# Kernel optimization log

Hardware: AMD Instinct MI355X
Metric: run time of the kernel (lower is better)

Reference implementation:

```python
import jax, jax.numpy as jnp
import numpy as np

NUM_HEADS = 4
HIDDEN = 128
LN_EPS = 1e-6
NEG_INF = -1e9


def setup_inputs() -> dict:
    key = jax.random.key(0)
    ks = jax.random.split(key, 8)
    B, S, H, NH = 64, 512, HIDDEN, NUM_HEADS
    enc = jax.random.normal(ks[0], (B, S, H), dtype=jnp.float32)
    mask = jax.random.randint(ks[1], (B, 1, S, S), 0, 2, dtype=jnp.int32)
    scale = 1.0 / np.sqrt(H)
    # torch Linear(H, H*NH, bias=False): weight is (H*NH, H); store transposed (H, H*NH)
    Wq = jax.random.normal(ks[2], (H, H * NH), dtype=jnp.float32) * scale
    Wk = jax.random.normal(ks[3], (H, H * NH), dtype=jnp.float32) * scale
    Wv = jax.random.normal(ks[4], (H, H * NH), dtype=jnp.float32) * scale
    Wo = jax.random.normal(ks[5], (H * NH, H), dtype=jnp.float32) * (1.0 / np.sqrt(H * NH))
    gamma = jnp.ones((H,), dtype=jnp.float32)
    beta = jnp.zeros((H,), dtype=jnp.float32)
    return {"enc": enc, "mask": mask, "Wq": Wq, "Wk": Wk, "Wv": Wv, "Wo": Wo, "gamma": gamma, "beta": beta}


def reference(enc, mask, Wq, Wk, Wv, Wo, gamma, beta):
    B, S, H = enc.shape
    NH = NUM_HEADS
    # projections -> (B, NH, S, H): each head has head_dim == hidden_units
    Q = (enc @ Wq).reshape(B, S, NH, H).transpose(0, 2, 1, 3)
    K = (enc @ Wk).reshape(B, S, NH, H).transpose(0, 2, 1, 3)
    V = (enc @ Wv).reshape(B, S, NH, H).transpose(0, 2, 1, 3)
    # scaled dot-product attention with mask (non-flash: full score matrix)
    scores = jnp.einsum('bhqd,bhkd->bhqk', Q, K) / jnp.sqrt(jnp.float32(H))
    scores = jnp.where(mask == 0, jnp.float32(NEG_INF), scores)
    attn = jax.nn.softmax(scores, axis=-1)  # dropout = identity in eval mode
    ctx = jnp.einsum('bhqk,bhkd->bhqd', attn, V)  # (B, NH, S, H)
    ctx = ctx.transpose(0, 2, 1, 3).reshape(B, S, NH * H)
    out = ctx @ Wo + enc  # dropout identity, residual add
    # LayerNorm over last dim
    mu = jnp.mean(out, axis=-1, keepdims=True)
    var = jnp.var(out, axis=-1, keepdims=True)
    return gamma * (out - mu) / jnp.sqrt(var + LN_EPS) + beta
```

## Files before the change

### kernel.cpp

```cpp
#include <hip/hip_runtime.h>
#include <stdint.h>

#define BATCH 64
#define SLEN 512
#define HID 128
#define NHEAD 4
#define DPROJ 512
#define MTOT (BATCH * SLEN)
#define SCALE 0.08838834764831845f
#define LOG2E 1.4426950408889634f

using short8 = __attribute__((ext_vector_type(8))) short;
using f32x4  = __attribute__((ext_vector_type(4))) float;
using u32x4  = __attribute__((ext_vector_type(4))) unsigned int;
using u32x2  = __attribute__((ext_vector_type(2))) unsigned int;
using us4    = __attribute__((ext_vector_type(4))) unsigned short;

__device__ __forceinline__ unsigned short f2bf(float f) {
  unsigned int u = __float_as_uint(f);
  u += 0x7fffu + ((u >> 16) & 1u);
  return (unsigned short)(u >> 16);
}

__global__ __launch_bounds__(256) void prep_kernel(
    const float* __restrict__ Wq,
    const float* __restrict__ Wk,
    const float* __restrict__ Wv,
    const float* __restrict__ Wo,
    const float* __restrict__ enc,
    const int* __restrict__ mask,
    unsigned short* __restrict__ WT,
    unsigned short* __restrict__ WoT,
    unsigned short* __restrict__ encb,
    unsigned int* __restrict__ mbits)
{
  if (blockIdx.x < 1024) {
    int idx = blockIdx.x * 256 + threadIdx.x;
    int z = idx >> 16;
    int i = idx & 65535;
    if (z < 3) {
      const float* W = (z == 0) ? Wq : (z == 1) ? Wk : Wv;
      float scale = (z == 0) ? (SCALE * LOG2E) : 1.0f;
      int k = i >> 9;
      int n = i & 511;
      WT[(size_t)z * 65536 + (size_t)n * 128 + k] = f2bf(W[i] * scale);
    } else {
      int k = i >> 7;
      int n = i & 127;
      WoT[(size_t)n * 512 + k] = f2bf(Wo[i]);
    }
  } else if (blockIdx.x < 3072) {
    size_t tid = (size_t)(blockIdx.x - 1024) * 256 + threadIdx.x;
    const float* s = enc + tid * 8;
    f32x4 a0 = *(const f32x4*)(s);
    f32x4 a1 = *(const f32x4*)(s + 4);
    short8 v;
    #pragma unroll
    for (int j = 0; j < 4; ++j) v[j] = (short)f2bf(a0[j]);
    #pragma unroll
    for (int j = 0; j < 4; ++j) v[4 + j] = (short)f2bf(a1[j]);
    *(short8*)(encb + tid * 8) = v;
  } else {
    const int l = threadIdx.x & 63;
    size_t wavebase = (size_t)(blockIdx.x - 3072) * 1024 + (threadIdx.x >> 6) * 256;
    unsigned long long b0 = __ballot(mask[wavebase + 0 * 64 + l] != 0);
    unsigned long long b1 = __ballot(mask[wavebase + 1 * 64 + l] != 0);
    unsigned long long b2 = __ballot(mask[wavebase + 2 * 64 + l] != 0);
    unsigned long long b3 = __ballot(mask[wavebase + 3 * 64 + l] != 0);
    if (l < 4) {
      unsigned long long v = (l & 2) ? ((l & 1) ? b3 : b2) : ((l & 1) ? b1 : b0);
      *(unsigned long long*)(mbits + (wavebase >> 5) + l * 2) = v;
    }
  }
}

__global__ __launch_bounds__(256) void qkv_kernel(
    const unsigned short* __restrict__ encb,
    const unsigned short* __restrict__ WT,
    unsigned short* __restrict__ Qh,
    unsigned short* __restrict__ Kh,
    unsigned short* __restrict__ Vt)
{
  const int nt = blockIdx.x;
  const int mt = blockIdx.y;
  const int t = threadIdx.x;
  const int lane = t & 63;
  const int w = t >> 6;
  const int quad = lane >> 4;
  const int l16 = lane & 15;

  __shared__ __align__(16) unsigned short Ald[128 * 136];
  __shared__ __align__(16) unsigned short Bld[2][128 * 72];

  const int m0 = mt * 128, n0 = nt * 128;
  const int wm = (w >> 1) * 64, wn = (w & 1) * 64;

  const int b_row = t >> 3, b_col = (t & 7) << 3;

  {
    u32x4 areg[8];
    #pragma unroll
    for (int i = 0; i < 8; ++i) {
      int idx = i * 256 + t;
      areg[i] = *(const u32x4*)(encb + (size_t)(m0 + (idx >> 4)) * HID + ((idx & 15) << 3));
    }
    u32x4 breg0[4];
    #pragma unroll
    for (int i = 0; i < 4; ++i)
      breg0[i] = *(const u32x4*)(WT + (size_t)(n0 + b_row + i * 32) * HID + b_col);
    #pragma unroll
    for (int i = 0; i < 8; ++i) {
      int idx = i * 256 + t;
      *(u32x4*)(Ald + (idx >> 4) * 136 + ((idx & 15) << 3)) = areg[i];
    }
    #pragma unroll
    for (int i = 0; i < 4; ++i)
      *(u32x4*)(Bld[0] + (b_row + i * 32) * 72 + b_col) = breg0[i];
  }
  u32x4 breg[4];
  #pragma unroll
  for (int i = 0; i < 4; ++i)
    breg[i] = *(const u32x4*)(WT + (size_t)(n0 + b_row + i * 32) * HID + 64 + b_col);
  asm volatile("s_waitcnt lgkmcnt(0)" ::: "memory");
  __builtin_amdgcn_s_barrier();

  f32x4 acc[4][4];
  #pragma unroll
  for (int s = 0; s < 6; ++s) {
    const int z = s >> 1, kc = s & 1, p = s & 1;
    if (kc == 0) {
      #pragma unroll
      for (int mi = 0; mi < 4; ++mi)
        #pragma unroll
        for (int ni = 0; ni < 4; ++ni)
          acc[mi][ni] = f32x4{0.f, 0.f, 0.f, 0.f};
    }

    const unsigned short* Br = Bld[p];
    #pragma unroll
    for (int kk = 0; kk < 2; ++kk) {
      short8 a[4], bb[4];
      #pragma unroll
      for (int mi = 0; mi < 4; ++mi)
        a[mi] = *(const short8*)(Ald + (wm + mi * 16 + l16) * 136 + kc * 64 + kk * 32 + quad * 8);
      #pragma unroll
      for (int ni = 0; ni < 4; ++ni)
        bb[ni] = *(const short8*)(Br + (wn + ni * 16 + l16) * 72 + kk * 32 + quad * 8);
      if (z < 2) {
        #pragma unroll
        for (int mi = 0; mi < 4; ++mi)
          #pragma unroll
          for (int ni = 0; ni < 4; ++ni)
            acc[mi][ni] = __builtin_amdgcn_mfma_f32_16x16x32_bf16(bb[ni], a[mi], acc[mi][ni], 0, 0, 0);
      } else {
        #pragma unroll
        for (int mi = 0; mi < 4; ++mi)
          #pragma unroll
          for (int ni = 0; ni < 4; ++ni)
            acc[mi][ni] = __builtin_amdgcn_mfma_f32_16x16x32_bf16(a[mi], bb[ni], acc[mi][ni], 0, 0, 0);
      }
    }

    if (s < 5) {
      unsigned short* Bw2 = Bld[p ^ 1];
      #pragma unroll
      for (int i = 0; i < 4; ++i)
        *(u32x4*)(Bw2 + (b_row + i * 32) * 72 + b_col) = breg[i];
      if (s < 4) {
        const int s2 = s + 2;
        const unsigned short* Wz = WT + (size_t)(s2 >> 1) * DPROJ * HID;
        #pragma unroll
        for (int i = 0; i < 4; ++i)
          breg[i] = *(const u32x4*)(Wz + (size_t)(n0 + b_row + i * 32) * HID + (s2 & 1) * 64 + b_col);
      }
      asm volatile("s_waitcnt lgkmcnt(0)" ::: "memory");
      __builtin_amdgcn_s_barrier();
    }

    if (kc == 1) {
      if (z < 2) {
        unsigned short* outz = ((z == 0) ? Qh : Kh) + (size_t)nt * MTOT * HID;
        #pragma unroll
        for (int mi = 0; mi < 4; ++mi)
          #pragma unroll
          for (int ni = 0; ni < 4; ++ni) {
            int m = m0 + wm + mi * 16 + l16;
            int dbase = wn + ni * 16 + quad * 4;
            us4 pk;
            #pragma unroll
            for (int r = 0; r < 4; ++r) pk[r] = f2bf(acc[mi][ni][r]);
            *(us4*)(outz + (size_t)m * HID + dbase) = pk;
          }
      } else {
        #pragma unroll
        for (int mi = 0; mi < 4; ++mi)
          #pragma unroll
          for (int ni = 0; ni < 4; ++ni) {
            int row0 = m0 + wm + mi * 16 + quad * 4;
            int b = row0 >> 9, sres = row0 & 511;
            int d = wn + ni * 16 + l16;
            us4 pk;
            #pragma unroll
            for (int r = 0; r < 4; ++r) pk[r] = f2bf(acc[mi][ni][r]);
            *(us4*)(Vt + ((size_t)(nt * BATCH + b) * HID + d) * SLEN + sres) = pk;
          }
      }
    }
  }
}

__global__ __launch_bounds__(512, 4) void attn_kernel(
    const unsigned short* __restrict__ Qh,
    const unsigned short* __restrict__ Kh,
    const unsigned short* __restrict__ Vt,
    const unsigned int* __restrict__ mbits,
    unsigned short* __restrict__ ctx)
{
  const int lin = blockIdx.x;
  const int work = (lin & 7) * 128 + (lin >> 3);
  const int qt = work & 3;
  const int h  = (work >> 2) & 3;
  const int b  = work >> 4;

  const int t = threadIdx.x;
  const int lane = t & 63;
  const int w = t >> 6;
  const int quad = lane >> 4;
  const int l16 = lane & 15;

  __shared__ __align__(16) unsigned short Kld[2][64 * 136];
  __shared__ __align__(16) unsigned short Vtld[2][128 * 72];

  const int q0 = qt * 128;
  const size_t rowbase = (size_t)b * SLEN;
  const unsigned short* kbase0 = Kh + ((size_t)h * MTOT + rowbase) * HID;
  const unsigned short* vbase  = Vt + (size_t)(h * BATCH + b) * HID * SLEN;
  const unsigned int* mrow = mbits + (size_t)b * SLEN * 16;

  const int k_key = t >> 4, k_col = (t & 15) << 3;
  const int v_d   = t >> 3, v_cc  = (t & 7) << 3;

  short8 qa[4];
  {
    const unsigned short* qbase =
        Qh + ((size_t)h * MTOT + rowbase + q0 + w * 16 + l16) * HID + quad * 8;
    #pragma unroll
    for (int kk = 0; kk < 4; ++kk)
      qa[kk] = *(const short8*)(qbase + kk * 32);
  }

  short8 ones;
  #pragma unroll
  for (int j = 0; j < 8; ++j) ones[j] = (short)0x3F80;

  f32x4 oc[8], oc9;
  #pragma unroll
  for (int nd = 0; nd < 8; ++nd) oc[nd] = f32x4{0.f, 0.f, 0.f, 0.f};
  oc9 = f32x4{0.f, 0.f, 0.f, 0.f};

  const unsigned int* mq = mrow + (size_t)(q0 + w * 16 + l16) * 16;

  u32x4 kreg[2], vreg[2];
  #pragma unroll
  for (int i = 0; i < 2; ++i) {
    kreg[i] = *(const u32x4*)(kbase0 + (size_t)(k_key + i * 32) * HID + k_col);
    vreg[i] = *(const u32x4*)(vbase + (size_t)(v_d + i * 64) * SLEN + v_cc);
  }
  #pragma unroll
  for (int i = 0; i < 2; ++i) {
    *(u32x4*)(Kld[0] + (k_key + i * 32) * 136 + k_col) = kreg[i];
    *(u32x4*)(Vtld[0] + (v_d + i * 64) * 72 + v_cc) = vreg[i];
  }
  #pragma unroll
  for (int i = 0; i < 2; ++i) {
    kreg[i] = *(const u32x4*)(kbase0 + (size_t)(64 + k_key + i * 32) * HID + k_col);
    vreg[i] = *(const u32x4*)(vbase + (size_t)(v_d + i * 64) * SLEN + 64 + v_cc);
  }
  asm volatile("s_waitcnt lgkmcnt(0)" ::: "memory");
  __builtin_amdgcn_s_barrier();

  for (int c0 = 0; c0 < SLEN; c0 += 64) {
    const int p = (c0 >> 6) & 1;
    const unsigned short* Kr = Kld[p];
    const unsigned short* Vr = Vtld[p];

    if (c0 + 64 < SLEN) {
      unsigned short* Kw = Kld[p ^ 1];
      unsigned short* Vw = Vtld[p ^ 1];
      #pragma unroll
      for (int i = 0; i < 2; ++i) {
        *(u32x4*)(Kw + (k_key + i * 32) * 136 + k_col) = kreg[i];
        *(u32x4*)(Vw + (v_d + i * 64) * 72 + v_cc) = vreg[i];
      }
      if (c0 + 128 < SLEN) {
        #pragma unroll
        for (int i = 0; i < 2; ++i) {
          kreg[i] = *(const u32x4*)(kbase0 + (size_t)(c0 + 128 + k_key + i * 32) * HID + k_col);
          vreg[i] = *(const u32x4*)(vbase + (size_t)(v_d + i * 64) * SLEN + c0 + 128 + v_cc);
        }
      }
    }

    u32x2 mw = *(const u32x2*)(mq + (c0 >> 5));

    f32x4 sc[4];
    #pragma unroll
    for (int ni = 0; ni < 4; ++ni) sc[ni] = f32x4{0.f, 0.f, 0.f, 0.f};
    __builtin_amdgcn_s_setprio(1);
    #pragma unroll
    for (int kk = 0; kk < 4; ++kk) {
      #pragma unroll
      for (int ni = 0; ni < 4; ++ni) {
        short8 bb = *(const short8*)(Kr + (ni * 16 + l16) * 136 + kk * 32 + quad * 8);
        sc[ni] = __builtin_amdgcn_mfma_f32_16x16x32_bf16(bb, qa[kk], sc[ni], 0, 0, 0);
      }
    }
    __builtin_amdgcn_s_setprio(0);

    unsigned int pk[4][2];
    #pragma unroll
    for (int ni = 0; ni < 4; ++ni) {
      unsigned wsel = (ni < 2) ? mw[0] : mw[1];
      float pp[4];
      #pragma unroll
      for (int r = 0; r < 4; ++r) {
        int bit = (ni & 1) * 16 + quad * 4 + r;
        float e = __builtin_amdgcn_exp2f(sc[ni][r]);
        pp[r] = ((wsel >> bit) & 1u) ? e : 0.f;
      }
      asm("v_cvt_pk_bf16_f32 %0, %1, %2" : "=v"(pk[ni][0]) : "v"(pp[0]), "v"(pp[1]));
      asm("v_cvt_pk_bf16_f32 %0, %1, %2" : "=v"(pk[ni][1]) : "v"(pp[2]), "v"(pp[3]));
    }

    #pragma unroll
    for (int kb = 0; kb < 2; ++kb) {
      unsigned int c0w = pk[kb * 2][0], c2w = pk[kb * 2 + 1][0];
      asm("v_permlane32_swap_b32 %0, %1" : "+v"(c0w), "+v"(c2w));
      asm("v_permlane16_swap_b32 %0, %1" : "+v"(c0w), "+v"(c2w));
      unsigned int c1w = pk[kb * 2][1], c3w = pk[kb * 2 + 1][1];
      asm("v_permlane32_swap_b32 %0, %1" : "+v"(c1w), "+v"(c3w));
      asm("v_permlane16_swap_b32 %0, %1" : "+v"(c1w), "+v"(c3w));
      short8 a = __builtin_bit_cast(short8, u32x4{c0w, c1w, c2w, c3w});
      __builtin_amdgcn_s_setprio(1);
      #pragma unroll
      for (int nd = 0; nd < 8; ++nd) {
        short8 bv = *(const short8*)(Vr + (nd * 16 + l16) * 72 + kb * 32 + quad * 8);
        oc[nd] = __builtin_amdgcn_mfma_f32_16x16x32_bf16(a, bv, oc[nd], 0, 0, 0);
      }
      oc9 = __builtin_amdgcn_mfma_f32_16x16x32_bf16(a, ones, oc9, 0, 0, 0);
      __builtin_amdgcn_s_setprio(0);
    }

    if (c0 + 64 < SLEN) {
      asm volatile("s_waitcnt lgkmcnt(0)" ::: "memory");
      __builtin_amdgcn_s_barrier();
    }
  }

  float rcp[4];
  #pragma unroll
  for (int r = 0; r < 4; ++r) rcp[r] = __builtin_amdgcn_rcpf(oc9[r]);
  #pragma unroll
  for (int nd = 0; nd < 8; ++nd)
    #pragma unroll
    for (int r = 0; r < 4; ++r) {
      float val = oc[nd][r] * rcp[r];
      int row = q0 + w * 16 + quad * 4 + r;
      int col = h * HID + nd * 16 + l16;
      ctx[(rowbase + row) * DPROJ + col] = f2bf(val);
    }
}

__global__ __launch_bounds__(256, 2) void oproj_ln_kernel(
    const unsigned short* __restrict__ ctx,
    const unsigned short* __restrict__ WoT,
    const float* __restrict__ enc,
    const float* __restrict__ gamma,
    const float* __restrict__ beta,
    float* __restrict__ out)
{
  const int m0 = blockIdx.x * 64;
  const int t = threadIdx.x;
  const int lane = t & 63;
  const int w = t >> 6;
  const int quad = lane >> 4;
  const int l16 = lane & 15;

  __shared__ __align__(16) unsigned short Actx[2][64 * 72];
  __shared__ __align__(16) unsigned short Bw[2][128 * 72];

  const int a_row = t >> 3, a_col = (t & 7) << 3;
  const int b_row = t >> 3, b_col = (t & 7) << 3;

  f32x4 acc[8];
  #pragma unroll
  for (int ni = 0; ni < 8; ++ni) acc[ni] = f32x4{0.f, 0.f, 0.f, 0.f};

  u32x4 areg[2], breg[4];
  #pragma unroll
  for (int i = 0; i < 2; ++i)
    areg[i] = *(const u32x4*)(ctx + (size_t)(m0 + a_row + i * 32) * DPROJ + a_col);
  #pragma unroll
  for (int i = 0; i < 4; ++i)
    breg[i] = *(const u32x4*)(WoT + (size_t)(b_row + i * 32) * DPROJ + b_col);
  #pragma unroll
  for (int i = 0; i < 2; ++i)
    *(u32x4*)(Actx[0] + (a_row + i * 32) * 72 + a_col) = areg[i];
  #pragma unroll
  for (int i = 0; i < 4; ++i)
    *(u32x4*)(Bw[0] + (b_row + i * 32) * 72 + b_col) = breg[i];
  #pragma unroll
  for (int i = 0; i < 2; ++i)
    areg[i] = *(const u32x4*)(ctx + (size_t)(m0 + a_row + i * 32) * DPROJ + 64 + a_col);
  #pragma unroll
  for (int i = 0; i < 4; ++i)
    breg[i] = *(const u32x4*)(WoT + (size_t)(b_row + i * 32) * DPROJ + 64 + b_col);
  asm volatile("s_waitcnt lgkmcnt(0)" ::: "memory");
  __builtin_amdgcn_s_barrier();

  #pragma unroll
  for (int it = 0; it < 8; ++it) {
    const int p = it & 1;
    const unsigned short* Ar = Actx[p];
    const unsigned short* Br = Bw[p];
    #pragma unroll
    for (int kk = 0; kk < 2; ++kk) {
      short8 a = *(const short8*)(Ar + (w * 16 + l16) * 72 + kk * 32 + quad * 8);
      #pragma unroll
      for (int ni = 0; ni < 8; ++ni) {
        short8 bb = *(const short8*)(Br + (ni * 16 + l16) * 72 + kk * 32 + quad * 8);
        acc[ni] = __builtin_amdgcn_mfma_f32_16x16x32_bf16(a, bb, acc[ni], 0, 0, 0);
      }
    }
    if (it < 7) {
      unsigned short* Aw2 = Actx[p ^ 1];
      unsigned short* Bw2 = Bw[p ^ 1];
      #pragma unroll
      for (int i = 0; i < 2; ++i)
        *(u32x4*)(Aw2 + (a_row + i * 32) * 72 + a_col) = areg[i];
      #pragma unroll
      for (int i = 0; i < 4; ++i)
        *(u32x4*)(Bw2 + (b_row + i * 32) * 72 + b_col) = breg[i];
      if (it < 6) {
        const int kc2 = (it + 2) * 64;
        #pragma unroll
        for (int i = 0; i < 2; ++i)
          areg[i] = *(const u32x4*)(ctx + (size_t)(m0 + a_row + i * 32) * DPROJ + kc2 + a_col);
        #pragma unroll
        for (int i = 0; i < 4; ++i)
          breg[i] = *(const u32x4*)(WoT + (size_t)(b_row + i * 32) * DPROJ + kc2 + b_col);
      }
      asm volatile("s_waitcnt lgkmcnt(0)" ::: "memory");
      __builtin_amdgcn_s_barrier();
    }
  }

  float g[8], be[8];
  #pragma unroll
  for (int ni = 0; ni < 8; ++ni) {
    g[ni] = gamma[ni * 16 + l16];
    be[ni] = beta[ni * 16 + l16];
  }

  float val[8][4];
  #pragma unroll
  for (int r = 0; r < 4; ++r) {
    int m = m0 + w * 16 + quad * 4 + r;
    const float* erow = enc + (size_t)m * HID;
    float s = 0.f, s2 = 0.f;
    #pragma unroll
    for (int ni = 0; ni < 8; ++ni) {
      float v = acc[ni][r] + erow[ni * 16 + l16];
      val[ni][r] = v;
      s += v;
      s2 += v * v;
    }
    #pragma unroll
    for (int off = 1; off < 16; off <<= 1) {
      s  += __shfl_xor(s, off, 64);
      s2 += __shfl_xor(s2, off, 64);
    }
    float mean = s * (1.f / 128.f);
    float var = s2 * (1.f / 128.f) - mean * mean;
    float rstd = rsqrtf(var + 1e-6f);
    float* orow = out + (size_t)m * HID;
    #pragma unroll
    for (int ni = 0; ni < 8; ++ni)
      orow[ni * 16 + l16] = g[ni] * (val[ni][r] - mean) * rstd + be[ni];
  }
}

extern "C" void kernel_launch(void* const* d_in, const int* in_sizes, int n_in,
                              void* d_out, int out_size, void* d_ws, size_t ws_size,
                              hipStream_t stream) {
  const float* enc   = (const float*)d_in[0];
  const int*   mask  = (const int*)d_in[1];
  const float* Wq    = (const float*)d_in[2];
  const float* Wk    = (const float*)d_in[3];
  const float* Wv    = (const float*)d_in[4];
  const float* Wo    = (const float*)d_in[5];
  const float* gamma = (const float*)d_in[6];
  const float* beta  = (const float*)d_in[7];
  float* out = (float*)d_out;

  unsigned short* WT  = (unsigned short*)d_ws;
  unsigned short* WoT = WT + (size_t)3 * DPROJ * HID;
  unsigned short* Qh  = WoT + (size_t)HID * DPROJ;
  unsigned short* Kh  = Qh + (size_t)NHEAD * MTOT * HID;
  unsigned short* Vt  = Kh + (size_t)NHEAD * MTOT * HID;
  unsigned short* ctx = Vt + (size_t)NHEAD * MTOT * HID;
  unsigned short* encb = ctx + (size_t)MTOT * DPROJ;
  unsigned int* mbits = (unsigned int*)(encb + (size_t)MTOT * HID * 2);

  prep_kernel<<<19456, 256, 0, stream>>>(Wq, Wk, Wv, Wo, enc, mask, WT, WoT, encb, mbits);
  qkv_kernel<<<dim3(4, 256), 256, 0, stream>>>(encb, WT, Qh, Kh, Vt);
  attn_kernel<<<1024, 512, 0, stream>>>(Qh, Kh, Vt, mbits, ctx);
  oproj_ln_kernel<<<MTOT / 64, 256, 0, stream>>>(ctx, WoT, enc, gamma, beta, out);
}
```

Before: 222.9 us.

## Fuse enc bf16 conversion and mask bit-packing into the QKV kernel

The fp32-to-bf16 conversion of enc now happens inside the QKV GEMM's A-tile load, so the intermediate encb buffer is no longer written and read back. Mask bit-packing moves into extra blocks of the QKV launch, with each block looping over 32 chunks. The prep kernel now only transposes the weights. This saves a round trip of enc through global memory and lets mask packing overlap with the GEMM, at the cost of reading fp32 enc (twice as many bytes) in each of the 4 n-tiles and making the mask blocks longer-running.

New measurement: 232.9 us. 4.5% more time.

```diff
diff --git a/kernel.cpp b/kernel.cpp
--- a/kernel.cpp
+++ b/kernel.cpp
@@ -27,63 +27,58 @@
     const float* __restrict__ Wk,
     const float* __restrict__ Wv,
     const float* __restrict__ Wo,
+    unsigned short* __restrict__ WT,
+    unsigned short* __restrict__ WoT)
+{
+  int idx = blockIdx.x * 256 + threadIdx.x;
+  int z = idx >> 16;
+  int i = idx & 65535;
+  if (z < 3) {
+    const float* W = (z == 0) ? Wq : (z == 1) ? Wk : Wv;
+    float scale = (z == 0) ? (SCALE * LOG2E) : 1.0f;
+    int k = i >> 9;
+    int n = i & 511;
+    WT[(size_t)z * 65536 + (size_t)n * 128 + k] = f2bf(W[i] * scale);
+  } else {
+    int k = i >> 7;
+    int n = i & 127;
+    WoT[(size_t)n * 512 + k] = f2bf(Wo[i]);
+  }
+}
+
+__global__ __launch_bounds__(256) void qkv_kernel(
     const float* __restrict__ enc,
     const int* __restrict__ mask,
-    unsigned short* __restrict__ WT,
-    unsigned short* __restrict__ WoT,
-    unsigned short* __restrict__ encb,
-    unsigned int* __restrict__ mbits)
-{
-  if (blockIdx.x < 1024) {
-    int idx = blockIdx.x * 256 + threadIdx.x;
-    int z = idx >> 16;
-    int i = idx & 65535;
-    if (z < 3) {
-      const float* W = (z == 0) ? Wq : (z == 1) ? Wk : Wv;
-      float scale = (z == 0) ? (SCALE * LOG2E) : 1.0f;
-      int k = i >> 9;
-      int n = i & 511;
-      WT[(size_t)z * 65536 + (size_t)n * 128 + k] = f2bf(W[i] * scale);
-    } else {
-      int k = i >> 7;
-      int n = i & 127;
-      WoT[(size_t)n * 512 + k] = f2bf(Wo[i]);
-    }
-  } else if (blockIdx.x < 3072) {
-    size_t tid = (size_t)(blockIdx.x - 1024) * 256 + threadIdx.x;
-    const float* s = enc + tid * 8;
-    f32x4 a0 = *(const f32x4*)(s);
-    f32x4 a1 = *(const f32x4*)(s + 4);
-    short8 v;
-    #pragma unroll
-    for (int j = 0; j < 4; ++j) v[j] = (short)f2bf(a0[j]);
-    #pragma unroll
-    for (int j = 0; j < 4; ++j) v[4 + j] = (short)f2bf(a1[j]);
-    *(short8*)(encb + tid * 8) = v;
-  } else {
-    const int l = threadIdx.x & 63;
-    size_t wavebase = (size_t)(blockIdx.x - 3072) * 1024 + (threadIdx.x >> 6) * 256;
-    unsigned long long b0 = __ballot(mask[wavebase + 0 * 64 + l] != 0);
-    unsigned long long b1 = __ballot(mask[wavebase + 1 * 64 + l] != 0);
-    unsigned long long b2 = __ballot(mask[wavebase + 2 * 64 + l] != 0);
-    unsigned long long b3 = __ballot(mask[wavebase + 3 * 64 + l] != 0);
-    if (l < 4) {
-      unsigned long long v = (l & 2) ? ((l & 1) ? b3 : b2) : ((l & 1) ? b1 : b0);
-      *(unsigned long long*)(mbits + (wavebase >> 5) + l * 2) = v;
-    }
-  }
-}
-
-__global__ __launch_bounds__(256) void qkv_kernel(
-    const unsigned short* __restrict__ encb,
     const unsigned short* __restrict__ WT,
     unsigned short* __restrict__ Qh,
     unsigned short* __restrict__ Kh,
-    unsigned short* __restrict__ Vt)
+    unsigned short* __restrict__ Vt,
+    unsigned int* __restrict__ mbits)
 {
-  const int nt = blockIdx.x;
-  const int mt = blockIdx.y;
+  const int bid = blockIdx.x;
   const int t = threadIdx.x;
+
+  if (bid >= 1024) {
+    const int l = t & 63;
+    const int wv = t >> 6;
+    #pragma unroll 4
+    for (int it = 0; it < 32; ++it) {
+      size_t vb = (size_t)(bid - 1024) * 32 + it;
+      size_t wavebase = vb * 1024 + (size_t)wv * 256;
+      unsigned long long b0 = __ballot(mask[wavebase + 0 * 64 + l] != 0);
+      unsigned long long b1 = __ballot(mask[wavebase + 1 * 64 + l] != 0);
+      unsigned long long b2 = __ballot(mask[wavebase + 2 * 64 + l] != 0);
+      unsigned long long b3 = __ballot(mask[wavebase + 3 * 64 + l] != 0);
+      if (l < 4) {
+        unsigned long long v = (l & 2) ? ((l & 1) ? b3 : b2) : ((l & 1) ? b1 : b0);
+        *(unsigned long long*)(mbits + (wavebase >> 5) + l * 2) = v;
+      }
+    }
+    return;
+  }
+
+  const int nt = bid & 3;
+  const int mt = bid >> 2;
   const int lane = t & 63;
   const int w = t >> 6;
   const int quad = lane >> 4;
@@ -98,20 +93,24 @@
   const int b_row = t >> 3, b_col = (t & 7) << 3;
 
   {
-    u32x4 areg[8];
+    u32x4 breg0[4];
+    #pragma unroll
+    for (int i = 0; i < 4; ++i)
+      breg0[i] = *(const u32x4*)(WT + (size_t)(n0 + b_row + i * 32) * HID + b_col);
     #pragma unroll
     for (int i = 0; i < 8; ++i) {
       int idx = i * 256 + t;
-      areg[i] = *(const u32x4*)(encb + (size_t)(m0 + (idx >> 4)) * HID + ((idx & 15) << 3));
-    }
-    u32x4 breg0[4];
-    #pragma unroll
-    for (int i = 0; i < 4; ++i)
-      breg0[i] = *(const u32x4*)(WT + (size_t)(n0 + b_row + i * 32) * HID + b_col);
-    #pragma unroll
-    for (int i = 0; i < 8; ++i) {
-      int idx = i * 256 + t;
-      *(u32x4*)(Ald + (idx >> 4) * 136 + ((idx & 15) << 3)) = areg[i];
+      int row = idx >> 4;
+      int col = (idx & 15) << 3;
+      const float* src = enc + (size_t)(m0 + row) * HID + col;
+      f32x4 a0 = *(const f32x4*)(src);
+      f32x4 a1 = *(const f32x4*)(src + 4);
+      short8 v;
+      #pragma unroll
+      for (int j = 0; j < 4; ++j) v[j] = (short)f2bf(a0[j]);
+      #pragma unroll
+      for (int j = 0; j < 4; ++j) v[4 + j] = (short)f2bf(a1[j]);
+      *(short8*)(Ald + row * 136 + col) = v;
     }
     #pragma unroll
     for (int i = 0; i < 4; ++i)
@@ -509,11 +508,10 @@
   unsigned short* Kh  = Qh + (size_t)NHEAD * MTOT * HID;
   unsigned short* Vt  = Kh + (size_t)NHEAD * MTOT * HID;
   unsigned short* ctx = Vt + (size_t)NHEAD * MTOT * HID;
-  unsigned short* encb = ctx + (size_t)MTOT * DPROJ;
-  unsigned int* mbits = (unsigned int*)(encb + (size_t)MTOT * HID * 2);
-
-  prep_kernel<<<19456, 256, 0, stream>>>(Wq, Wk, Wv, Wo, enc, mask, WT, WoT, encb, mbits);
-  qkv_kernel<<<dim3(4, 256), 256, 0, stream>>>(encb, WT, Qh, Kh, Vt);
+  unsigned int* mbits = (unsigned int*)(ctx + (size_t)MTOT * DPROJ);
+
+  prep_kernel<<<1024, 256, 0, stream>>>(Wq, Wk, Wv, Wo, WT, WoT);
+  qkv_kernel<<<1536, 256, 0, stream>>>(enc, mask, WT, Qh, Kh, Vt, mbits);
   attn_kernel<<<1024, 512, 0, stream>>>(Qh, Kh, Vt, mbits, ctx);
   oproj_ln_kernel<<<MTOT / 64, 256, 0, stream>>>(ctx, WoT, enc, gamma, beta, out);
 }
```
